# Kernel optimization log

Measured on AMD Instinct MI355X. Metric: run time of the kernel, lower is better.

## Reference

```python
import jax, jax.numpy as jnp
import numpy as np

E = 8388608          # total edges across batch
G = 2048             # num_graphs
LARGE_NEG = -1.0e9
SCORE_EPS = 1e-6     # self.score_eps
STOP_BIAS = 0.0      # self.stop_logit_bias
RAND_PROB = 0.1      # self.random_action_prob (training)
TEMP = 1.0           # policy_temperature (>= MIN_TEMPERATURE)
PROB_EPS = 1e-12
EPS = float(np.finfo(np.float32).eps)  # torch.finfo(edge_tokens.dtype).eps


def setup_inputs() -> dict:
    key = jax.random.key(0)
    k1, k2, k3, k4, k5 = jax.random.split(key, 5)
    edge_scores = jax.random.uniform(k1, (E,), dtype=jnp.float32)
    edge_residual = jax.random.normal(k2, (E,), dtype=jnp.float32)
    stop_residual = jax.random.normal(k3, (G,), dtype=jnp.float32)
    valid_edges = jax.random.bernoulli(k4, 0.9, (E,))
    edge_batch = jnp.sort(jax.random.randint(k5, (E,), 0, G, dtype=jnp.int32))
    return {"edge_scores": edge_scores, "edge_residual": edge_residual,
            "stop_residual": stop_residual, "valid_edges": valid_edges,
            "edge_batch": edge_batch}


def _segment_log_probs(edge_logits, stop_logits, valid, edge_batch, temp):
    """Faithful port of _log_probs_from_logits: per-graph stable softmax over
    a ragged set of edge logits plus one stop logit per graph."""
    masked = jnp.where(valid, edge_logits, LARGE_NEG)
    scaled = masked / temp                                   # [E]
    sstop = stop_logits / temp                               # [G]
    max_edge = jax.ops.segment_max(scaled, edge_batch, num_segments=G)
    has_edge = jax.ops.segment_sum(jnp.ones_like(scaled), edge_batch, num_segments=G) > 0
    max_edge = jnp.where(has_edge, max_edge, LARGE_NEG)
    max_joint = jnp.maximum(max_edge, sstop)                 # [G]
    exp_edges = jax.ops.segment_sum(jnp.exp(scaled - max_joint[edge_batch]),
                                    edge_batch, num_segments=G)
    exp_stop = jnp.exp(sstop - max_joint)
    log_denom = max_joint + jnp.log(exp_edges + exp_stop + EPS)  # [G]
    log_edge = jnp.where(valid, scaled - log_denom[edge_batch], LARGE_NEG)
    log_stop = sstop - log_denom
    return log_edge, log_stop


def reference(edge_scores, edge_residual, stop_residual, valid_edges, edge_batch):
    # base (prior) distribution from GNN edge scores + stop bias
    base_edge_logits = jnp.log(jnp.maximum(edge_scores, SCORE_EPS))
    base_stop_logits = jnp.full((G,), STOP_BIAS, dtype=jnp.float32)
    base_log_edge, base_log_stop = _segment_log_probs(
        base_edge_logits, base_stop_logits, valid_edges, edge_batch, 1.0)
    # combine with policy residuals and renormalize at temperature
    combined_edge = base_log_edge + edge_residual
    combined_stop = base_log_stop + stop_residual
    clean_log_edge, clean_log_stop = _segment_log_probs(
        combined_edge, combined_stop, valid_edges, edge_batch, TEMP)
    clean_edge_prob = jnp.exp(clean_log_edge)
    clean_stop_prob = jnp.exp(clean_log_stop)
    # uniform random-action mixing
    valid_counts = jax.ops.segment_sum(valid_edges.astype(jnp.float32),
                                       edge_batch, num_segments=G)
    total_actions = jnp.maximum(valid_counts + 1.0, 1.0)     # [G]
    uniform_edge = jnp.where(valid_edges, 1.0 / total_actions[edge_batch], 0.0)
    uniform_stop = 1.0 / total_actions
    sample_edge = (1.0 - RAND_PROB) * clean_edge_prob + RAND_PROB * uniform_edge
    sample_stop = (1.0 - RAND_PROB) * clean_stop_prob + RAND_PROB * uniform_stop
    log_sample_edge = jnp.where(valid_edges,
                                jnp.log(jnp.maximum(sample_edge, PROB_EPS)),
                                LARGE_NEG)
    log_sample_stop = jnp.log(jnp.maximum(sample_stop, PROB_EPS))
    # greedy action per graph: best edge vs stop
    best_val = jax.ops.segment_max(log_sample_edge, edge_batch, num_segments=G)
    idx = jnp.arange(E, dtype=jnp.int32)
    cand = jnp.where(log_sample_edge == best_val[edge_batch], idx, E)
    best_idx = jax.ops.segment_min(cand, edge_batch, num_segments=G)   # [G]
    counts = jax.ops.segment_sum(jnp.ones((E,), jnp.int32), edge_batch, num_segments=G)
    stop_indices = jnp.cumsum(counts)                         # edge_ptr[1:]
    take_stop = log_sample_stop >= best_val
    actions = jnp.where(take_stop, stop_indices, best_idx)
    chosen_edge_lp = clean_log_edge[jnp.minimum(best_idx, E - 1)]
    log_pf = jnp.where(take_stop, clean_log_stop, chosen_edge_lp)     # [G]
    return clean_log_edge, clean_log_stop, actions, log_pf
```

## Files before the change

kernel.cpp:

```cpp
#include <hip/hip_runtime.h>
#include <math.h>
#include <climits>

#define BLOCK 256
#define NCHUNK 5
#define REGCAP (NCHUNK * 1024)
#define LARGE_NEG (-1.0e9f)
#define SCORE_EPS 1e-6f
#define RANDP 0.1f
#define PROB_EPS 1e-12f
#define F32EPS 1.1920928955078125e-7f

__global__ void gfn_setup(const int* __restrict__ batch, int E, int G,
                          int* __restrict__ ptr,
                          const unsigned int* __restrict__ vwords, int nwords,
                          int nbytes, int* __restrict__ flag, int nbPtr) {
  if ((int)blockIdx.x < nbPtr) {
    int g = blockIdx.x * BLOCK + threadIdx.x;
    if (g > G) return;
    long long ghat = (long long)g * (long long)E / (long long)(G > 0 ? G : 1);
    long long wlo = ghat - 16384, whi = ghat + 16384;
    int lo = wlo > 0 ? (int)wlo : 0;
    int hi = whi < (long long)E ? (int)whi : E;
    while (lo < hi) {
      int mid = (lo + hi) >> 1;
      if (batch[mid] < g) lo = mid + 1; else hi = mid;
    }
    int r = lo;
    bool ok = (r == 0 || batch[r - 1] < g) && (r == E || batch[r] >= g);
    if (!ok) {
      lo = 0; hi = E;
      while (lo < hi) {
        int mid = (lo + hi) >> 1;
        if (batch[mid] < g) lo = mid + 1; else hi = mid;
      }
      r = lo;
    }
    ptr[g] = r;
  } else {
    int c = 0;
    for (int i = threadIdx.x; i < nwords; i += BLOCK) {
      unsigned int w = vwords[i];
      c += ((w & 0x000000FFu) != 0) + ((w & 0x0000FF00u) != 0) +
           ((w & 0x00FF0000u) != 0) + ((w & 0xFF000000u) != 0);
    }
#pragma unroll
    for (int o = 32; o >= 1; o >>= 1) c += __shfl_xor(c, o);
    __shared__ int part[4];
    if ((threadIdx.x & 63) == 0) part[threadIdx.x >> 6] = c;
    __syncthreads();
    if (threadIdx.x == 0) {
      int t = part[0] + part[1] + part[2] + part[3];
      flag[0] = (2 * t > nbytes) ? 1 : 0;
    }
  }
}

__global__ __launch_bounds__(BLOCK) void
gfn_main(const float* __restrict__ scores,
         const float* __restrict__ resid,
         const float* __restrict__ stop_resid,
         const void* __restrict__ validp,
         const int* __restrict__ ptr,
         const int* __restrict__ flag,
         float* __restrict__ out, int E, int G) {
  __shared__ float redf[24];
  __shared__ int redi[4];

  const int g = blockIdx.x;
  const int start = ptr[g];
  const int end = ptr[g + 1];
  const bool byteFmt = (flag[0] != 0);
  const unsigned char* vb = (const unsigned char*)validp;
  const int* vi = (const int*)validp;
  const int abase = start & ~3;
  const int wid = (int)(threadIdx.x >> 6);
  const int lane = (int)(threadIdx.x & 63);

  if ((E & 3) == 0 && (end - abase) <= REGCAP) {
    const int t4 = (int)threadIdx.x * 4;
    float c[NCHUNK][4];
    float smax = 0.f, ssum = 0.f;
    int vcnt = 0;
    float om = LARGE_NEG, os = 0.f;
    float bv = -INFINITY;
    int bi = INT_MAX;

#pragma unroll
    for (int j = 0; j < NCHUNK; ++j) {
      const int e0 = abase + j * 1024 + t4;
      if (e0 < end) {
        const float4 s4 = *(const float4*)(scores + e0);
        const float4 r4 = *(const float4*)(resid + e0);
        unsigned int m;
        if (byteFmt) {
          const unsigned int u = *(const unsigned int*)(vb + e0);
          m = ((u & 0x000000FFu) ? 1u : 0u) | ((u & 0x0000FF00u) ? 2u : 0u) |
              ((u & 0x00FF0000u) ? 4u : 0u) | ((u & 0xFF000000u) ? 8u : 0u);
        } else {
          const int4 u = *(const int4*)(vi + e0);
          m = (u.x ? 1u : 0u) | (u.y ? 2u : 0u) | (u.z ? 4u : 0u) | (u.w ? 8u : 0u);
        }
        const float ss[4] = {s4.x, s4.y, s4.z, s4.w};
        const float rr[4] = {r4.x, r4.y, r4.z, r4.w};
#pragma unroll
        for (int k = 0; k < 4; ++k) {
          const int e = e0 + k;
          const bool ok = ((m >> k) & 1u) && (e >= start) && (e < end);
          float t = LARGE_NEG;
          if (ok) {
            const float w = fmaxf(ss[k], SCORE_EPS);
            smax = fmaxf(smax, w);
            ssum += w;
            ++vcnt;
            t = __logf(w) + rr[k];
            if (t > om) {
              os = os * __expf(om - t) + 1.f;
              om = t;
            } else {
              os += __expf(t - om);
            }
            if (t > bv || (t == bv && e < bi)) { bv = t; bi = e; }
          }
          c[j][k] = t;
        }
      } else {
#pragma unroll
        for (int k = 0; k < 4; ++k) c[j][k] = LARGE_NEG;
      }
    }

#pragma unroll
    for (int o = 32; o >= 1; o >>= 1) {
      smax = fmaxf(smax, __shfl_xor(smax, o));
      ssum += __shfl_xor(ssum, o);
      vcnt += __shfl_xor(vcnt, o);
      const float m2v = __shfl_xor(om, o);
      const float s2v = __shfl_xor(os, o);
      const float nm = fmaxf(om, m2v);
      os = os * __expf(om - nm) + s2v * __expf(m2v - nm);
      om = nm;
      const float v2 = __shfl_xor(bv, o);
      const int i2 = __shfl_xor(bi, o);
      if (v2 > bv || (v2 == bv && i2 < bi)) { bv = v2; bi = i2; }
    }
    if (lane == 0) {
      redf[wid] = smax; redf[4 + wid] = ssum; redf[8 + wid] = (float)vcnt;
      redf[12 + wid] = om; redf[16 + wid] = os; redf[20 + wid] = bv;
      redi[wid] = bi;
    }
    __syncthreads();
    smax = fmaxf(fmaxf(redf[0], redf[1]), fmaxf(redf[2], redf[3]));
    ssum = (redf[4] + redf[5]) + (redf[6] + redf[7]);
    const float vc = (redf[8] + redf[9]) + (redf[10] + redf[11]);
    om = redf[12]; os = redf[16];
#pragma unroll
    for (int w = 1; w < 4; ++w) {
      const float mb = redf[12 + w], sb = redf[16 + w];
      const float nm = fmaxf(om, mb);
      os = os * __expf(om - nm) + sb * __expf(mb - nm);
      om = nm;
    }
    bv = redf[20]; bi = redi[0];
#pragma unroll
    for (int w = 1; w < 4; ++w) {
      const float v2 = redf[20 + w]; const int i2 = redi[w];
      if (v2 > bv || (v2 == bv && i2 < bi)) { bv = v2; bi = i2; }
    }

    const float M = fmaxf(smax, 1.f);
    const float invM = 1.f / M;
    const float ld1 = __logf(M) + __logf(ssum * invM + invM + F32EPS);
    const float m2 = om - ld1;
    const float ss2 = stop_resid[g] - ld1;
    const float mj2 = fmaxf(m2, ss2);
    const float s2 = os * __expf(m2 - mj2);
    const float ld2 = mj2 + __logf(s2 + __expf(ss2 - mj2) + F32EPS);
    const float clean_stop = ss2 - ld2;
    const float invt = 1.f / fmaxf(vc + 1.f, 1.f);
    const float off3 = ld1 + ld2;

#pragma unroll
    for (int j = 0; j < NCHUNK; ++j) {
      const int e0 = abase + j * 1024 + t4;
      if (e0 < end) {
        float ov[4];
#pragma unroll
        for (int k = 0; k < 4; ++k) {
          const float t = c[j][k];
          ov[k] = (t != LARGE_NEG) ? (t - off3) : LARGE_NEG;
        }
        if (e0 >= start && e0 + 4 <= end) {
          *(float4*)(out + e0) = make_float4(ov[0], ov[1], ov[2], ov[3]);
        } else {
#pragma unroll
          for (int k = 0; k < 4; ++k) {
            const int e = e0 + k;
            if (e >= start && e < end) out[e] = ov[k];
          }
        }
      }
    }
    if (threadIdx.x == 0) {
      const bool anyvalid = (bi != INT_MAX);
      const float wclean = bv - off3;
      float bvls = LARGE_NEG;
      if (anyvalid) {
        const float p = (1.f - RANDP) * __expf(wclean) + RANDP * invt;
        bvls = __logf(fmaxf(p, PROB_EPS));
      }
      const float ssp = (1.f - RANDP) * __expf(clean_stop) + RANDP * invt;
      const float lss = __logf(fmaxf(ssp, PROB_EPS));
      const bool take_stop = (lss >= bvls);
      out[E + g]         = clean_stop;
      out[E + G + g]     = take_stop ? (float)end : (float)bi;
      out[E + 2 * G + g] = take_stop ? clean_stop : wclean;
    }
    return;
  }

  const int n = end - start;
  auto load_l = [&](int e) -> float {
    float s = scores[e];
    int v = byteFmt ? (int)vb[e] : vi[e];
    return v ? __logf(fmaxf(s, SCORE_EPS)) : LARGE_NEG;
  };

  float m1 = LARGE_NEG, vc = 0.f;
  for (int i = threadIdx.x; i < n; i += BLOCK) {
    float l = load_l(start + i);
    m1 = fmaxf(m1, l);
    if (l != LARGE_NEG) vc += 1.f;
  }
#pragma unroll
  for (int o = 32; o >= 1; o >>= 1) {
    m1 = fmaxf(m1, __shfl_xor(m1, o));
    vc += __shfl_xor(vc, o);
  }
  if (lane == 0) { redf[wid] = m1; redf[4 + wid] = vc; }
  __syncthreads();
  m1 = fmaxf(fmaxf(redf[0], redf[1]), fmaxf(redf[2], redf[3]));
  vc = (redf[4] + redf[5]) + (redf[6] + redf[7]);
  __syncthreads();

  const float mj1 = fmaxf(m1, 0.f);
  float s1 = 0.f;
  for (int i = threadIdx.x; i < n; i += BLOCK)
    s1 += __expf(load_l(start + i) - mj1);
#pragma unroll
  for (int o = 32; o >= 1; o >>= 1) s1 += __shfl_xor(s1, o);
  if (lane == 0) redf[wid] = s1;
  __syncthreads();
  s1 = (redf[0] + redf[1]) + (redf[2] + redf[3]);
  __syncthreads();
  const float ld1 = mj1 + __logf(s1 + __expf(-mj1) + F32EPS);

  float m2 = LARGE_NEG;
  for (int i = threadIdx.x; i < n; i += BLOCK) {
    float l = load_l(start + i);
    float cc = (l != LARGE_NEG) ? (l - ld1 + resid[start + i]) : LARGE_NEG;
    m2 = fmaxf(m2, cc);
  }
#pragma unroll
  for (int o = 32; o >= 1; o >>= 1) m2 = fmaxf(m2, __shfl_xor(m2, o));
  if (lane == 0) redf[wid] = m2;
  __syncthreads();
  m2 = fmaxf(fmaxf(redf[0], redf[1]), fmaxf(redf[2], redf[3]));
  __syncthreads();

  const float ss2 = stop_resid[g] - ld1;
  const float mj2 = fmaxf(m2, ss2);
  float s2 = 0.f;
  for (int i = threadIdx.x; i < n; i += BLOCK) {
    float l = load_l(start + i);
    float cc = (l != LARGE_NEG) ? (l - ld1 + resid[start + i]) : LARGE_NEG;
    s2 += __expf(cc - mj2);
  }
#pragma unroll
  for (int o = 32; o >= 1; o >>= 1) s2 += __shfl_xor(s2, o);
  if (lane == 0) redf[wid] = s2;
  __syncthreads();
  s2 = (redf[0] + redf[1]) + (redf[2] + redf[3]);
  __syncthreads();
  const float ld2 = mj2 + __logf(s2 + __expf(ss2 - mj2) + F32EPS);
  const float clean_stop = ss2 - ld2;
  const float invt = 1.f / fmaxf(vc + 1.f, 1.f);

  float bv = -INFINITY; int bi = INT_MAX; float bc = 0.f;
  for (int i = threadIdx.x; i < n; i += BLOCK) {
    const int e = start + i;
    float l = load_l(e);
    float cc = (l != LARGE_NEG) ? (l - ld1 + resid[e]) : LARGE_NEG;
    const bool v = (cc != LARGE_NEG);
    const float clean = cc - ld2;
    out[e] = v ? clean : LARGE_NEG;
    float ls;
    if (v) {
      const float p = (1.f - RANDP) * __expf(clean) + RANDP * invt;
      ls = __logf(fmaxf(p, PROB_EPS));
    } else ls = LARGE_NEG;
    if (ls > bv || (ls == bv && e < bi)) { bv = ls; bi = e; bc = clean; }
  }
#pragma unroll
  for (int o = 32; o >= 1; o >>= 1) {
    const float v2 = __shfl_xor(bv, o);
    const int i2 = __shfl_xor(bi, o);
    const float c2 = __shfl_xor(bc, o);
    if (v2 > bv || (v2 == bv && i2 < bi)) { bv = v2; bi = i2; bc = c2; }
  }
  if (lane == 0) { redf[wid] = bv; redf[4 + wid] = bc; redi[wid] = bi; }
  __syncthreads();
  if (threadIdx.x == 0) {
    bv = redf[0]; bi = redi[0]; bc = redf[4];
    for (int w = 1; w < 4; ++w) {
      if (redf[w] > bv || (redf[w] == bv && redi[w] < bi)) {
        bv = redf[w]; bi = redi[w]; bc = redf[4 + w];
      }
    }
    const float ssp = (1.f - RANDP) * __expf(clean_stop) + RANDP * invt;
    const float lss = __logf(fmaxf(ssp, PROB_EPS));
    const bool take_stop = (lss >= bv);
    out[E + g]         = clean_stop;
    out[E + G + g]     = take_stop ? (float)end : (float)bi;
    out[E + 2 * G + g] = take_stop ? clean_stop : bc;
  }
}

extern "C" void kernel_launch(void* const* d_in, const int* in_sizes, int n_in,
                              void* d_out, int out_size, void* d_ws, size_t ws_size,
                              hipStream_t stream) {
  const float* scores     = (const float*)d_in[0];
  const float* resid      = (const float*)d_in[1];
  const float* stop_resid = (const float*)d_in[2];
  const void*  validp     = d_in[3];
  const int*   batch      = (const int*)d_in[4];
  const int E = in_sizes[0];
  const int G = in_sizes[2];

  int* flag = (int*)d_ws;
  int* ptr  = (int*)d_ws + 64;
  float* out = (float*)d_out;

  int sample_bytes = (E < 8192) ? (E & ~3) : 8192;
  int nbPtr = (G + 1 + BLOCK - 1) / BLOCK;
  gfn_setup<<<nbPtr + 1, BLOCK, 0, stream>>>(batch, E, G, ptr,
                                             (const unsigned int*)validp,
                                             sample_bytes / 4, sample_bytes,
                                             flag, nbPtr);
  gfn_main<<<G, BLOCK, 0, stream>>>(scores, resid, stop_resid, validp, ptr,
                                    flag, out, E, G);
}
```

Measured before the change: 37.96 us.

## Fuse segment-pointer search and valid-format detection into main kernel

After: 33.24 us. 12.4% less time.

```diff
diff --git a/kernel.cpp b/kernel.cpp
--- a/kernel.cpp
+++ b/kernel.cpp
@@ -11,49 +11,27 @@
 #define PROB_EPS 1e-12f
 #define F32EPS 1.1920928955078125e-7f
 
-__global__ void gfn_setup(const int* __restrict__ batch, int E, int G,
-                          int* __restrict__ ptr,
-                          const unsigned int* __restrict__ vwords, int nwords,
-                          int nbytes, int* __restrict__ flag, int nbPtr) {
-  if ((int)blockIdx.x < nbPtr) {
-    int g = blockIdx.x * BLOCK + threadIdx.x;
-    if (g > G) return;
-    long long ghat = (long long)g * (long long)E / (long long)(G > 0 ? G : 1);
-    long long wlo = ghat - 16384, whi = ghat + 16384;
-    int lo = wlo > 0 ? (int)wlo : 0;
-    int hi = whi < (long long)E ? (int)whi : E;
+__device__ __forceinline__ int scalar_lb(const int* __restrict__ batch,
+                                         int E, int G, int target) {
+  const long long ghat =
+      (long long)target * (long long)E / (long long)(G > 0 ? G : 1);
+  long long wlo = ghat - 16384, whi = ghat + 16384;
+  int lo = wlo > 0 ? (int)wlo : 0;
+  int hi = whi < (long long)E ? (int)whi : E;
+  while (lo < hi) {
+    const int mid = (lo + hi) >> 1;
+    if (batch[mid] < target) lo = mid + 1; else hi = mid;
+  }
+  bool ok = (lo == 0 || batch[lo - 1] < target) &&
+            (lo == E || batch[lo] >= target);
+  if (!ok) {
+    lo = 0; hi = E;
     while (lo < hi) {
-      int mid = (lo + hi) >> 1;
-      if (batch[mid] < g) lo = mid + 1; else hi = mid;
-    }
-    int r = lo;
-    bool ok = (r == 0 || batch[r - 1] < g) && (r == E || batch[r] >= g);
-    if (!ok) {
-      lo = 0; hi = E;
-      while (lo < hi) {
-        int mid = (lo + hi) >> 1;
-        if (batch[mid] < g) lo = mid + 1; else hi = mid;
-      }
-      r = lo;
-    }
-    ptr[g] = r;
-  } else {
-    int c = 0;
-    for (int i = threadIdx.x; i < nwords; i += BLOCK) {
-      unsigned int w = vwords[i];
-      c += ((w & 0x000000FFu) != 0) + ((w & 0x0000FF00u) != 0) +
-           ((w & 0x00FF0000u) != 0) + ((w & 0xFF000000u) != 0);
-    }
-#pragma unroll
-    for (int o = 32; o >= 1; o >>= 1) c += __shfl_xor(c, o);
-    __shared__ int part[4];
-    if ((threadIdx.x & 63) == 0) part[threadIdx.x >> 6] = c;
-    __syncthreads();
-    if (threadIdx.x == 0) {
-      int t = part[0] + part[1] + part[2] + part[3];
-      flag[0] = (2 * t > nbytes) ? 1 : 0;
-    }
-  }
+      const int mid = (lo + hi) >> 1;
+      if (batch[mid] < target) lo = mid + 1; else hi = mid;
+    }
+  }
+  return lo;
 }
 
 __global__ __launch_bounds__(BLOCK) void
@@ -61,21 +39,42 @@
          const float* __restrict__ resid,
          const float* __restrict__ stop_resid,
          const void* __restrict__ validp,
-         const int* __restrict__ ptr,
-         const int* __restrict__ flag,
+         const int* __restrict__ batch,
          float* __restrict__ out, int E, int G) {
   __shared__ float redf[24];
   __shared__ int redi[4];
+  __shared__ int sb[2];
+  __shared__ int sflag;
 
   const int g = blockIdx.x;
-  const int start = ptr[g];
-  const int end = ptr[g + 1];
-  const bool byteFmt = (flag[0] != 0);
   const unsigned char* vb = (const unsigned char*)validp;
   const int* vi = (const int*)validp;
-  const int abase = start & ~3;
   const int wid = (int)(threadIdx.x >> 6);
   const int lane = (int)(threadIdx.x & 63);
+
+  if (threadIdx.x == 0) {
+    sb[0] = scalar_lb(batch, E, G, g);
+  } else if (threadIdx.x == 64) {
+    sb[1] = scalar_lb(batch, E, G, g + 1);
+  } else if (wid == 2) {
+    const unsigned int* vwords = (const unsigned int*)validp;
+    const int sampleBytes = (E < 1024) ? (E & ~3) : 1024;
+    const int nwords = sampleBytes >> 2;
+    int cnt = 0;
+    for (int w = lane; w < nwords; w += 64) {
+      const unsigned int x = vwords[w];
+      cnt += ((x & 0x000000FFu) != 0) + ((x & 0x0000FF00u) != 0) +
+             ((x & 0x00FF0000u) != 0) + ((x & 0xFF000000u) != 0);
+    }
+#pragma unroll
+    for (int o = 32; o >= 1; o >>= 1) cnt += __shfl_xor(cnt, o);
+    if (lane == 0) sflag = (2 * cnt > sampleBytes) ? 1 : 0;
+  }
+  __syncthreads();
+  const int start = sb[0];
+  const int end = sb[1];
+  const bool byteFmt = (sflag != 0);
+  const int abase = start & ~3;
 
   if ((E & 3) == 0 && (end - abase) <= REGCAP) {
     const int t4 = (int)threadIdx.x * 4;
@@ -114,12 +113,9 @@
             ssum += w;
             ++vcnt;
             t = __logf(w) + rr[k];
-            if (t > om) {
-              os = os * __expf(om - t) + 1.f;
-              om = t;
-            } else {
-              os += __expf(t - om);
-            }
+            const float nm = fmaxf(om, t);
+            os = os * __expf(om - nm) + __expf(t - nm);
+            om = nm;
             if (t > bv || (t == bv && e < bi)) { bv = t; bi = e; }
           }
           c[j][k] = t;
@@ -156,9 +152,9 @@
     om = redf[12]; os = redf[16];
 #pragma unroll
     for (int w = 1; w < 4; ++w) {
-      const float mb = redf[12 + w], sb = redf[16 + w];
+      const float mb = redf[12 + w], sb2 = redf[16 + w];
       const float nm = fmaxf(om, mb);
-      os = os * __expf(om - nm) + sb * __expf(mb - nm);
+      os = os * __expf(om - nm) + sb2 * __expf(mb - nm);
       om = nm;
     }
     bv = redf[20]; bi = redi[0];
@@ -337,16 +333,6 @@
   const int E = in_sizes[0];
   const int G = in_sizes[2];
 
-  int* flag = (int*)d_ws;
-  int* ptr  = (int*)d_ws + 64;
-  float* out = (float*)d_out;
-
-  int sample_bytes = (E < 8192) ? (E & ~3) : 8192;
-  int nbPtr = (G + 1 + BLOCK - 1) / BLOCK;
-  gfn_setup<<<nbPtr + 1, BLOCK, 0, stream>>>(batch, E, G, ptr,
-                                             (const unsigned int*)validp,
-                                             sample_bytes / 4, sample_bytes,
-                                             flag, nbPtr);
-  gfn_main<<<G, BLOCK, 0, stream>>>(scores, resid, stop_resid, validp, ptr,
-                                    flag, out, E, G);
+  gfn_main<<<G, BLOCK, 0, stream>>>(scores, resid, stop_resid, validp, batch,
+                                    (float*)d_out, E, G);
 }
```
